# Optimization experiments

Hardware: AMD Instinct MI355X
Metric: run time of the kernel (lower is better)

The kernel has to match this reference:

```python
import jax, jax.numpy as jnp
import numpy as np

N = 100000   # nodes
E = 1000000  # directed edges
D = 64       # in_dim
H = 64       # hid_dim
O = 64       # out_dim


def _lin_init(key, fan_in, fan_out):
    # torch nn.Linear default init: U(-1/sqrt(fan_in), 1/sqrt(fan_in))
    k1, k2 = jax.random.split(key)
    s = 1.0 / np.sqrt(fan_in)
    W = jax.random.uniform(k1, (fan_in, fan_out), jnp.float32, -s, s)
    b = jax.random.uniform(k2, (fan_out,), jnp.float32, -s, s)
    return W, b


def setup_inputs() -> dict:
    key = jax.random.key(0)
    ks = jax.random.split(key, 6)
    x = jax.random.normal(ks[0], (N, D), jnp.float32)
    src = jax.random.randint(ks[1], (E,), 0, N)
    dst = jax.random.randint(ks[2], (E,), 0, N)
    W1, b1 = _lin_init(ks[3], 2 * D, H)
    W2, b2 = _lin_init(ks[4], 2 * H, H)
    W3, b3 = _lin_init(ks[5], 2 * H, O)
    return {"x": x, "src": src, "dst": dst,
            "W1": W1, "b1": b1, "W2": W2, "b2": b2, "W3": W3, "b3": b3}


def _graphconv_left(x, s, d, n):
    # DGL GraphConv(norm='left', weight=False, bias=False):
    # divide src features by src out-degree (clamped min 1), sum at dst.
    deg = jax.ops.segment_sum(jnp.ones_like(s, x.dtype), s, num_segments=n)
    deg = jnp.maximum(deg, 1.0)
    msg = (x / deg[:, None])[s]                       # [E, F] gather
    return jax.ops.segment_sum(msg, d, num_segments=n)  # [N, F] scatter-add


def _sage_layer(x, s, d, n, W, b, use_activation):
    agg = _graphconv_left(x, s, d, n)
    h = jnp.concatenate([x, agg], axis=1) @ W + b
    return jax.nn.relu(h) if use_activation else h


def reference(x, src, dst, W1, b1, W2, b2, W3, b3):
    n = x.shape[0]
    # dir_seq = 'OIU': out-edges, reversed edges, undirected (both directions)
    usrc = jnp.concatenate([src, dst])
    udst = jnp.concatenate([dst, src])
    x = _sage_layer(x, src, dst, n, W1, b1, True)    # 'O'
    x = _sage_layer(x, dst, src, n, W2, b2, True)    # 'I' (reverse graph)
    x = _sage_layer(x, usrc, udst, n, W3, b3, False) # 'U' (undirected)
    return x
```

## Files before the change

### kernel.cpp

```cpp
#include <hip/hip_runtime.h>
#include <hip/hip_fp16.h>


#define BSHIFT 10
#define BMASK  ((1 << BSHIFT) - 1)
#define NBMAX  128
#define PCHUNK 2048
#define HCHUNK 4096

__global__ __launch_bounds__(256) void bucket_hist_k(
    const int* __restrict__ src, const int* __restrict__ dst,
    int* __restrict__ bcnt_out, int* __restrict__ bcnt_in, int E) {
    __shared__ int h0[NBMAX], h1[NBMAX];
    const int t = threadIdx.x;
    const int e0 = blockIdx.x * HCHUNK;
    int n = E - e0; if (n > HCHUNK) n = HCHUNK;
    for (int i = t; i < NBMAX; i += 256) { h0[i] = 0; h1[i] = 0; }
    __syncthreads();
    for (int i = t; i < n; i += 256) {
        atomicAdd(&h0[src[e0 + i] >> BSHIFT], 1);
        atomicAdd(&h1[dst[e0 + i] >> BSHIFT], 1);
    }
    __syncthreads();
    if (t < NBMAX) {
        int c = h0[t];
        if (c) atomicAdd(&bcnt_out[t], c);
    } else {
        int b = t - NBMAX;
        int c = h1[b];
        if (c) atomicAdd(&bcnt_in[b], c);
    }
}

__global__ void bucket_scan_k(const int* __restrict__ bcnt_out, const int* __restrict__ bcnt_in,
                              int* __restrict__ bip_out, int* __restrict__ bip_in,
                              int* __restrict__ bcur_out, int* __restrict__ bcur_in, int NB) {
    __shared__ int s[1024];
    int t = threadIdx.x;
#pragma unroll 1
    for (int pass = 0; pass < 2; ++pass) {
        const int* bcnt = pass ? bcnt_in : bcnt_out;
        int* bip = pass ? bip_in : bip_out;
        int* bcur = pass ? bcur_in : bcur_out;
        int v = (t < NB) ? bcnt[t] : 0;
        s[t] = v; __syncthreads();
        for (int off = 1; off < 1024; off <<= 1) {
            int x = (t >= off) ? s[t - off] : 0;
            __syncthreads();
            s[t] += x;
            __syncthreads();
        }
        int excl = s[t] - v;
        if (t < NB) { bip[t] = excl; bcur[t] = excl; }
        if (t == NB) bip[NB] = excl;
        __syncthreads();
    }
}

__global__ __launch_bounds__(256) void partition_k(
    const int* __restrict__ src, const int* __restrict__ dst,
    int* __restrict__ bcur_out, int* __restrict__ bcur_in,
    unsigned* __restrict__ part_out, unsigned* __restrict__ part_in, int E) {
    __shared__ int sS[PCHUNK], sD[PCHUNK];
    __shared__ int hist[2][NBMAX];
    __shared__ int gbase[2][NBMAX];
    const int t = threadIdx.x;
    const int e0 = blockIdx.x * PCHUNK;
    int n = E - e0; if (n > PCHUNK) n = PCHUNK;

    for (int i = t; i < NBMAX; i += 256) { hist[0][i] = 0; hist[1][i] = 0; }
    __syncthreads();
    for (int i = t; i < n; i += 256) {
        int s = src[e0 + i], d = dst[e0 + i];
        sS[i] = s; sD[i] = d;
        atomicAdd(&hist[0][d >> BSHIFT], 1);
        atomicAdd(&hist[1][s >> BSHIFT], 1);
    }
    __syncthreads();
    if (t < NBMAX) {
        int c = hist[0][t];
        gbase[0][t] = c ? atomicAdd(&bcur_in[t], c) : 0;
        hist[0][t] = 0;
    } else {
        int b = t - NBMAX;
        int c = hist[1][b];
        gbase[1][b] = c ? atomicAdd(&bcur_out[b], c) : 0;
        hist[1][b] = 0;
    }
    __syncthreads();
    for (int i = t; i < n; i += 256) {
        int s = sS[i], d = sD[i];
        int bi = d >> BSHIFT;
        int p = gbase[0][bi] + atomicAdd(&hist[0][bi], 1);
        part_in[p] = ((unsigned)s << BSHIFT) | (unsigned)(d & BMASK);
        int bo = s >> BSHIFT;
        int q = gbase[1][bo] + atomicAdd(&hist[1][bo], 1);
        part_out[q] = ((unsigned)d << BSHIFT) | (unsigned)(s & BMASK);
    }
}

__global__ __launch_bounds__(1024) void bucket_sort_k(
    const unsigned* __restrict__ pa, const int* __restrict__ bipa,
    const unsigned* __restrict__ pb, const int* __restrict__ bipb,
    int* __restrict__ ipa, int* __restrict__ ipb,
    int* __restrict__ cola, int* __restrict__ colb,
    int* __restrict__ dega, int* __restrict__ degb, int N, int E) {
    const unsigned* part = blockIdx.y ? pb : pa;
    const int* bip = blockIdx.y ? bipb : bipa;
    int* ip  = blockIdx.y ? ipb : ipa;
    int* col = blockIdx.y ? colb : cola;
    int* deg = blockIdx.y ? degb : dega;
    __shared__ int cnt[1024];
    __shared__ int s[1024];
    const int g = blockIdx.x, t = threadIdx.x;
    const int b = bip[g], e = bip[g + 1];

    cnt[t] = 0;
    __syncthreads();
    for (int i = b + t; i < e; i += 1024) atomicAdd(&cnt[part[i] & (unsigned)BMASK], 1);
    __syncthreads();

    int v = cnt[t];
    s[t] = v;
    __syncthreads();
    for (int off = 1; off < 1024; off <<= 1) {
        int x = (t >= off) ? s[t - off] : 0;
        __syncthreads();
        s[t] += x;
        __syncthreads();
    }
    int base = b + s[t] - v;
    int node = (g << BSHIFT) + t;
    if (node < N) { ip[node] = base; deg[node] = v; }
    cnt[t] = base;
    if (g == 0 && t == 0) ip[N] = E;
    __syncthreads();
    for (int i = b + t; i < e; i += 1024) {
        unsigned rec = part[i];
        int p = atomicAdd(&cnt[rec & (unsigned)BMASK], 1);
        col[p] = (int)((rec >> BSHIFT) << 7);
    }
}

__global__ void scale_rows_k(const float* __restrict__ in, const int* __restrict__ deg,
                             __half* __restrict__ out, int n4) {
    int t = blockIdx.x * blockDim.x + threadIdx.x;
    if (t < n4) {
        int m = deg[t >> 4];
        float s = 1.0f / (float)(m < 1 ? 1 : m);
        float4 v = ((const float4*)in)[t];
        __half2 p01 = __floats2half2_rn(v.x * s, v.y * s);
        __half2 p23 = __floats2half2_rn(v.z * s, v.w * s);
        uint2 u;
        u.x = *(unsigned*)&p01;
        u.y = *(unsigned*)&p23;
        *(uint2*)(out + ((size_t)t << 2)) = u;
    }
}

__device__ __forceinline__ void acc_row(float4& acc, uint2 u) {
    __half2 h01 = *(__half2*)&u.x, h23 = *(__half2*)&u.y;
    acc.x += __low2float(h01); acc.y += __high2float(h01);
    acc.z += __low2float(h23); acc.w += __high2float(h23);
}

__device__ __forceinline__ void agg_list(const char* __restrict__ hsb,
                                         const int* __restrict__ col,
                                         int b, int e, int lane, int grp, int fo8,
                                         float4& a0, float4& a1, float4& a2, float4& a3) {
    for (int base = b; base < e; base += 64) {
        int cnt = e - base; if (cnt > 64) cnt = 64;
        int my = (lane < cnt) ? col[base + lane] : 0;
        for (int j = 0; j < cnt; j += 16) {
            int i0 = j + grp, i1 = j + 4 + grp, i2 = j + 8 + grp, i3 = j + 12 + grp;
            int o0 = __shfl(my, i0 < cnt ? i0 : 0);
            int o1 = __shfl(my, i1 < cnt ? i1 : 0);
            int o2 = __shfl(my, i2 < cnt ? i2 : 0);
            int o3 = __shfl(my, i3 < cnt ? i3 : 0);
            uint2 u0 = *(const uint2*)(hsb + o0 + fo8);
            uint2 u1 = *(const uint2*)(hsb + o1 + fo8);
            uint2 u2 = *(const uint2*)(hsb + o2 + fo8);
            uint2 u3 = *(const uint2*)(hsb + o3 + fo8);
            if (i0 < cnt) acc_row(a0, u0);
            if (i1 < cnt) acc_row(a1, u1);
            if (i2 < cnt) acc_row(a2, u2);
            if (i3 < cnt) acc_row(a3, u3);
        }
    }
}

__device__ __forceinline__ void agg_finish(float4 a0, float4 a1, float4 a2, float4 a3,
                                           float* __restrict__ agg, int node,
                                           int lane, int fo) {
    float4 acc;
    acc.x = (a0.x + a1.x) + (a2.x + a3.x);
    acc.y = (a0.y + a1.y) + (a2.y + a3.y);
    acc.z = (a0.z + a1.z) + (a2.z + a3.z);
    acc.w = (a0.w + a1.w) + (a2.w + a3.w);
    acc.x += __shfl_xor(acc.x, 16); acc.y += __shfl_xor(acc.y, 16);
    acc.z += __shfl_xor(acc.z, 16); acc.w += __shfl_xor(acc.w, 16);
    acc.x += __shfl_xor(acc.x, 32); acc.y += __shfl_xor(acc.y, 32);
    acc.z += __shfl_xor(acc.z, 32); acc.w += __shfl_xor(acc.w, 32);
    if (lane < 16) ((float4*)(agg + ((size_t)node << 6)))[fo] = acc;
}

__global__ void agg_k(const __half* __restrict__ hs, const int* __restrict__ ip,
                      const int* __restrict__ col, float* __restrict__ agg, int N) {
    int node = (blockIdx.x * blockDim.x + threadIdx.x) >> 6;
    int lane = threadIdx.x & 63;
    if (node >= N) return;
    const int grp = lane >> 4, fo = lane & 15, fo8 = fo << 3;
    float4 z = make_float4(0.f, 0.f, 0.f, 0.f);
    float4 a0 = z, a1 = z, a2 = z, a3 = z;
    agg_list((const char*)hs, col, ip[node], ip[node + 1], lane, grp, fo8, a0, a1, a2, a3);
    agg_finish(a0, a1, a2, a3, agg, node, lane, fo);
}

__global__ void agg_dual_k(const __half* __restrict__ hs,
                           const int* __restrict__ ipA, const int* __restrict__ colA,
                           const int* __restrict__ ipB, const int* __restrict__ colB,
                           float* __restrict__ agg, int N) {
    int node = (blockIdx.x * blockDim.x + threadIdx.x) >> 6;
    int lane = threadIdx.x & 63;
    if (node >= N) return;
    const int grp = lane >> 4, fo = lane & 15, fo8 = fo << 3;
    float4 z = make_float4(0.f, 0.f, 0.f, 0.f);
    float4 a0 = z, a1 = z, a2 = z, a3 = z;
    agg_list((const char*)hs, colA, ipA[node], ipA[node + 1], lane, grp, fo8, a0, a1, a2, a3);
    agg_list((const char*)hs, colB, ipB[node], ipB[node + 1], lane, grp, fo8, a0, a1, a2, a3);
    agg_finish(a0, a1, a2, a3, agg, node, lane, fo);
}

template <bool RELU, bool WRITE_HS, bool DEG2>
__global__ __launch_bounds__(256, 2) void gemm_cat_k(
    const float* X, const float* A,
    const float* __restrict__ W, const float* __restrict__ B,
    const int* __restrict__ dga, const int* __restrict__ dgb,
    __half* __restrict__ hs_out, float* out, int N) {
    __shared__ float sW[128 * 64];
    __shared__ float sX[64 * 64];
    __shared__ float sA[64 * 64];
    const int tid = threadIdx.x;

    for (int i = tid; i < 2048; i += 256) ((float4*)sW)[i] = ((const float4*)W)[i];

    const int row0 = blockIdx.x * 64;
    for (int i = tid; i < 1024; i += 256) {
        int r = i >> 4, c4 = (i & 15) << 2;
        int gr = row0 + r;
        float4 xv = make_float4(0.f, 0.f, 0.f, 0.f), av = xv;
        if (gr < N) {
            xv = ((const float4*)X)[(size_t)gr * 16 + (i & 15)];
            av = ((const float4*)A)[(size_t)gr * 16 + (i & 15)];
        }
        int sc = c4 ^ ((r & 12) << 1);
        *(float4*)&sX[(r << 6) + sc] = xv;
        *(float4*)&sA[(r << 6) + sc] = av;
    }
    __syncthreads();

    const int c0 = (tid & 15) << 2;
    const int r0 = (tid >> 4) << 2;
    const int sw = (r0 & 12) << 1;

    float4 bv = *(const float4*)(B + c0);
    float acc[4][4];
#pragma unroll
    for (int i = 0; i < 4; ++i) {
        acc[i][0] = bv.x; acc[i][1] = bv.y; acc[i][2] = bv.z; acc[i][3] = bv.w;
    }

#define GEMM_ROW(i, av)                                                       \
    acc[i][0] = fmaf(av.x, w0.x, acc[i][0]); acc[i][1] = fmaf(av.x, w0.y, acc[i][1]); \
    acc[i][2] = fmaf(av.x, w0.z, acc[i][2]); acc[i][3] = fmaf(av.x, w0.w, acc[i][3]); \
    acc[i][0] = fmaf(av.y, w1.x, acc[i][0]); acc[i][1] = fmaf(av.y, w1.y, acc[i][1]); \
    acc[i][2] = fmaf(av.y, w1.z, acc[i][2]); acc[i][3] = fmaf(av.y, w1.w, acc[i][3]); \
    acc[i][0] = fmaf(av.z, w2.x, acc[i][0]); acc[i][1] = fmaf(av.z, w2.y, acc[i][1]); \
    acc[i][2] = fmaf(av.z, w2.z, acc[i][2]); acc[i][3] = fmaf(av.z, w2.w, acc[i][3]); \
    acc[i][0] = fmaf(av.w, w3.x, acc[i][0]); acc[i][1] = fmaf(av.w, w3.y, acc[i][1]); \
    acc[i][2] = fmaf(av.w, w3.z, acc[i][2]); acc[i][3] = fmaf(av.w, w3.w, acc[i][3]);

#pragma unroll 4
    for (int kb = 0; kb < 64; kb += 4) {
        const int kx = kb ^ sw;
        float4 w0 = *(const float4*)&sW[((kb + 0) << 6) + c0];
        float4 w1 = *(const float4*)&sW[((kb + 1) << 6) + c0];
        float4 w2 = *(const float4*)&sW[((kb + 2) << 6) + c0];
        float4 w3 = *(const float4*)&sW[((kb + 3) << 6) + c0];
        float4 a0 = *(const float4*)&sX[((r0 + 0) << 6) + kx];
        float4 a1 = *(const float4*)&sX[((r0 + 1) << 6) + kx];
        float4 a2 = *(const float4*)&sX[((r0 + 2) << 6) + kx];
        float4 a3 = *(const float4*)&sX[((r0 + 3) << 6) + kx];
        GEMM_ROW(0, a0) GEMM_ROW(1, a1) GEMM_ROW(2, a2) GEMM_ROW(3, a3)
    }
#pragma unroll 4
    for (int kb = 0; kb < 64; kb += 4) {
        const int kx = kb ^ sw;
        float4 w0 = *(const float4*)&sW[((kb + 64) << 6) + c0];
        float4 w1 = *(const float4*)&sW[((kb + 65) << 6) + c0];
        float4 w2 = *(const float4*)&sW[((kb + 66) << 6) + c0];
        float4 w3 = *(const float4*)&sW[((kb + 67) << 6) + c0];
        float4 a0 = *(const float4*)&sA[((r0 + 0) << 6) + kx];
        float4 a1 = *(const float4*)&sA[((r0 + 1) << 6) + kx];
        float4 a2 = *(const float4*)&sA[((r0 + 2) << 6) + kx];
        float4 a3 = *(const float4*)&sA[((r0 + 3) << 6) + kx];
        GEMM_ROW(0, a0) GEMM_ROW(1, a1) GEMM_ROW(2, a2) GEMM_ROW(3, a3)
    }
#undef GEMM_ROW

#pragma unroll
    for (int i = 0; i < 4; ++i) {
        int gr = row0 + r0 + i;
        if (gr < N) {
            float4 o;
            o.x = RELU ? fmaxf(acc[i][0], 0.f) : acc[i][0];
            o.y = RELU ? fmaxf(acc[i][1], 0.f) : acc[i][1];
            o.z = RELU ? fmaxf(acc[i][2], 0.f) : acc[i][2];
            o.w = RELU ? fmaxf(acc[i][3], 0.f) : acc[i][3];
            *(float4*)(out + ((size_t)gr << 6) + c0) = o;
            if (WRITE_HS) {
                int m = dga[gr] + (DEG2 ? dgb[gr] : 0);
                float rr = 1.0f / (float)(m < 1 ? 1 : m);
                __half2 p01 = __floats2half2_rn(o.x * rr, o.y * rr);
                __half2 p23 = __floats2half2_rn(o.z * rr, o.w * rr);
                uint2 u;
                u.x = *(unsigned*)&p01;
                u.y = *(unsigned*)&p23;
                *(uint2*)(hs_out + ((size_t)gr << 6) + c0) = u;
            }
        }
    }
}

extern "C" void kernel_launch(void* const* d_in, const int* in_sizes, int n_in,
                              void* d_out, int out_size, void* d_ws, size_t ws_size,
                              hipStream_t stream) {
    const float* x  = (const float*)d_in[0];
    const int* src  = (const int*)d_in[1];
    const int* dst  = (const int*)d_in[2];
    const float* W1 = (const float*)d_in[3];
    const float* b1 = (const float*)d_in[4];
    const float* W2 = (const float*)d_in[5];
    const float* b2 = (const float*)d_in[6];
    const float* W3 = (const float*)d_in[7];
    const float* b3 = (const float*)d_in[8];

    const int N = in_sizes[0] / 64;
    const int E = in_sizes[1];
    const int NB = (N + BMASK) >> BSHIFT;

    float* bufH  = (float*)d_ws;
    __half* bufHS = (__half*)(bufH + (size_t)N * 64);
    int* deg_out = (int*)(bufHS + (size_t)N * 64);
    int* deg_in  = deg_out + N;
    int* ip_out  = deg_in + N;
    int* ip_in   = ip_out + (N + 1);
    int* bcnt_out = ip_in + (N + 1);
    int* bcnt_in  = bcnt_out + NB;
    int* bip_out  = bcnt_in + NB;
    int* bip_in   = bip_out + (NB + 1);
    int* bcur_out = bip_in + (NB + 1);
    int* bcur_in  = bcur_out + NB;
    unsigned* part_out = (unsigned*)(bcur_in + NB);
    unsigned* part_in  = part_out + E;
    int* col_out = (int*)(part_in + E);
    int* col_in  = col_out + E;

    float* aggB = (float*)d_out;

    const int TPB = 256;
    const int n4  = N * 16;
    const int g4  = (n4 + TPB - 1) / TPB;
    const int gAg = (int)(((size_t)N * 64 + TPB - 1) / TPB);
    const int gGm = (N + 63) / 64;
    const int gP  = (E + PCHUNK - 1) / PCHUNK;
    const int gH  = (E + HCHUNK - 1) / HCHUNK;

    hipMemsetAsync(bcnt_out, 0, 2 * (size_t)NB * sizeof(int), stream);
    bucket_hist_k<<<gH, TPB, 0, stream>>>(src, dst, bcnt_out, bcnt_in, E);
    bucket_scan_k<<<1, 1024, 0, stream>>>(bcnt_out, bcnt_in, bip_out, bip_in,
                                          bcur_out, bcur_in, NB);
    partition_k<<<gP, TPB, 0, stream>>>(src, dst, bcur_out, bcur_in,
                                        part_out, part_in, E);
    bucket_sort_k<<<dim3(NB, 2), 1024, 0, stream>>>(part_out, bip_out, part_in, bip_in,
                                                    ip_out, ip_in, col_out, col_in,
                                                    deg_out, deg_in, N, E);

    scale_rows_k<<<g4, TPB, 0, stream>>>(x, deg_out, bufHS, n4);
    agg_k<<<gAg, TPB, 0, stream>>>(bufHS, ip_in, col_in, aggB, N);
    gemm_cat_k<true, true, false><<<gGm, TPB, 0, stream>>>(x, aggB, W1, b1,
                                                           deg_in, nullptr, bufHS, bufH, N);

    agg_k<<<gAg, TPB, 0, stream>>>(bufHS, ip_out, col_out, aggB, N);
    gemm_cat_k<true, true, true><<<gGm, TPB, 0, stream>>>(bufH, aggB, W2, b2,
                                                          deg_in, deg_out, bufHS, bufH, N);

    agg_dual_k<<<gAg, TPB, 0, stream>>>(bufHS, ip_in, col_in, ip_out, col_out, aggB, N);
    gemm_cat_k<false, false, false><<<gGm, TPB, 0, stream>>>(bufH, aggB, W3, b3,
                                                             nullptr, nullptr, nullptr,
                                                             (float*)d_out, N);
}
```

Baseline: 293.9 us.

## Replace FP32 SIMT concat-GEMM with FP16 MFMA kernel and prepacked weights

Swaps the shared-memory FP32 FMA GEMM for a wave-level MFMA 16x16x32 fp16 kernel. A new prep kernel converts each weight matrix to fp16 once per call and packs it in the MFMA B-fragment layout, and each wave loads its A fragments straight from global memory with no LDS. The aim is to cut the ALU cost of the three dense layers. In exchange, inputs and weights are rounded to fp16, and the output stores become scalar and strided across lanes, which may hurt write coalescing.

```diff
diff --git a/kernel.cpp b/kernel.cpp
--- a/kernel.cpp
+++ b/kernel.cpp
@@ -7,6 +7,9 @@
 #define NBMAX  128
 #define PCHUNK 2048
 #define HCHUNK 4096
+
+typedef _Float16 half8 __attribute__((ext_vector_type(8)));
+typedef float floatx4 __attribute__((ext_vector_type(4)));
 
 __global__ __launch_bounds__(256) void bucket_hist_k(
     const int* __restrict__ src, const int* __restrict__ dst,
@@ -142,6 +145,21 @@
     }
 }
 
+__global__ void prep_w_k(const float* __restrict__ W1, const float* __restrict__ W2,
+                         const float* __restrict__ W3, __half* __restrict__ wt) {
+    const float* W = blockIdx.x == 0 ? W1 : (blockIdx.x == 1 ? W2 : W3);
+    __half* o = wt + (size_t)blockIdx.x * 8192;
+    for (int idx = threadIdx.x; idx < 8192; idx += 256) {
+        int j = idx & 7;
+        int l = (idx >> 3) & 63;
+        int f = idx >> 9;
+        int kq = f >> 2, ct = f & 3;
+        int k = (kq << 5) + ((l >> 4) << 3) + j;
+        int c = (ct << 4) + (l & 15);
+        o[idx] = __float2half(W[k * 64 + c]);
+    }
+}
+
 __global__ void scale_rows_k(const float* __restrict__ in, const int* __restrict__ deg,
                              __half* __restrict__ out, int n4) {
     int t = blockIdx.x * blockDim.x + threadIdx.x;
@@ -232,101 +250,72 @@
 }
 
 template <bool RELU, bool WRITE_HS, bool DEG2>
-__global__ __launch_bounds__(256, 2) void gemm_cat_k(
-    const float* X, const float* A,
-    const float* __restrict__ W, const float* __restrict__ B,
+__global__ __launch_bounds__(256) void gemm_mfma_k(
+    const float* X, const float* A, const __half* __restrict__ WT,
+    const float* __restrict__ B,
     const int* __restrict__ dga, const int* __restrict__ dgb,
     __half* __restrict__ hs_out, float* out, int N) {
-    __shared__ float sW[128 * 64];
-    __shared__ float sX[64 * 64];
-    __shared__ float sA[64 * 64];
     const int tid = threadIdx.x;
-
-    for (int i = tid; i < 2048; i += 256) ((float4*)sW)[i] = ((const float4*)W)[i];
-
-    const int row0 = blockIdx.x * 64;
-    for (int i = tid; i < 1024; i += 256) {
-        int r = i >> 4, c4 = (i & 15) << 2;
-        int gr = row0 + r;
-        float4 xv = make_float4(0.f, 0.f, 0.f, 0.f), av = xv;
-        if (gr < N) {
-            xv = ((const float4*)X)[(size_t)gr * 16 + (i & 15)];
-            av = ((const float4*)A)[(size_t)gr * 16 + (i & 15)];
+    const int w = tid >> 6, l = tid & 63;
+    const int lr = l & 15, lh = l >> 4;
+    const int row0 = blockIdx.x * 64 + (w << 4);
+    const int arow = row0 + lr;
+    const bool rok = arow < N;
+
+    half8 bf[4][4];
+#pragma unroll
+    for (int kq = 0; kq < 4; ++kq)
+#pragma unroll
+        for (int ct = 0; ct < 4; ++ct)
+            bf[kq][ct] = *(const half8*)(WT + ((((kq << 2) | ct) << 9) + (l << 3)));
+
+    half8 af[4];
+#pragma unroll
+    for (int kq = 0; kq < 4; ++kq) {
+        const float* src = (kq < 2) ? X : A;
+        int kbase = ((kq & 1) << 5) + (lh << 3);
+        float4 v0 = make_float4(0.f, 0.f, 0.f, 0.f), v1 = v0;
+        if (rok) {
+            v0 = *(const float4*)(src + ((size_t)arow << 6) + kbase);
+            v1 = *(const float4*)(src + ((size_t)arow << 6) + kbase + 4);
         }
-        int sc = c4 ^ ((r & 12) << 1);
-        *(float4*)&sX[(r << 6) + sc] = xv;
-        *(float4*)&sA[(r << 6) + sc] = av;
-    }
-    __syncthreads();
-
-    const int c0 = (tid & 15) << 2;
-    const int r0 = (tid >> 4) << 2;
-    const int sw = (r0 & 12) << 1;
-
-    float4 bv = *(const float4*)(B + c0);
-    float acc[4][4];
-#pragma unroll
-    for (int i = 0; i < 4; ++i) {
-        acc[i][0] = bv.x; acc[i][1] = bv.y; acc[i][2] = bv.z; acc[i][3] = bv.w;
-    }
-
-#define GEMM_ROW(i, av)                                                       \
-    acc[i][0] = fmaf(av.x, w0.x, acc[i][0]); acc[i][1] = fmaf(av.x, w0.y, acc[i][1]); \
-    acc[i][2] = fmaf(av.x, w0.z, acc[i][2]); acc[i][3] = fmaf(av.x, w0.w, acc[i][3]); \
-    acc[i][0] = fmaf(av.y, w1.x, acc[i][0]); acc[i][1] = fmaf(av.y, w1.y, acc[i][1]); \
-    acc[i][2] = fmaf(av.y, w1.z, acc[i][2]); acc[i][3] = fmaf(av.y, w1.w, acc[i][3]); \
-    acc[i][0] = fmaf(av.z, w2.x, acc[i][0]); acc[i][1] = fmaf(av.z, w2.y, acc[i][1]); \
-    acc[i][2] = fmaf(av.z, w2.z, acc[i][2]); acc[i][3] = fmaf(av.z, w2.w, acc[i][3]); \
-    acc[i][0] = fmaf(av.w, w3.x, acc[i][0]); acc[i][1] = fmaf(av.w, w3.y, acc[i][1]); \
-    acc[i][2] = fmaf(av.w, w3.z, acc[i][2]); acc[i][3] = fmaf(av.w, w3.w, acc[i][3]);
-
-#pragma unroll 4
-    for (int kb = 0; kb < 64; kb += 4) {
-        const int kx = kb ^ sw;
-        float4 w0 = *(const float4*)&sW[((kb + 0) << 6) + c0];
-        float4 w1 = *(const float4*)&sW[((kb + 1) << 6) + c0];
-        float4 w2 = *(const float4*)&sW[((kb + 2) << 6) + c0];
-        float4 w3 = *(const float4*)&sW[((kb + 3) << 6) + c0];
-        float4 a0 = *(const float4*)&sX[((r0 + 0) << 6) + kx];
-        float4 a1 = *(const float4*)&sX[((r0 + 1) << 6) + kx];
-        float4 a2 = *(const float4*)&sX[((r0 + 2) << 6) + kx];
-        float4 a3 = *(const float4*)&sX[((r0 + 3) << 6) + kx];
-        GEMM_ROW(0, a0) GEMM_ROW(1, a1) GEMM_ROW(2, a2) GEMM_ROW(3, a3)
-    }
-#pragma unroll 4
-    for (int kb = 0; kb < 64; kb += 4) {
-        const int kx = kb ^ sw;
-        float4 w0 = *(const float4*)&sW[((kb + 64) << 6) + c0];
-        float4 w1 = *(const float4*)&sW[((kb + 65) << 6) + c0];
-        float4 w2 = *(const float4*)&sW[((kb + 66) << 6) + c0];
-        float4 w3 = *(const float4*)&sW[((kb + 67) << 6) + c0];
-        float4 a0 = *(const float4*)&sA[((r0 + 0) << 6) + kx];
-        float4 a1 = *(const float4*)&sA[((r0 + 1) << 6) + kx];
-        float4 a2 = *(const float4*)&sA[((r0 + 2) << 6) + kx];
-        float4 a3 = *(const float4*)&sA[((r0 + 3) << 6) + kx];
-        GEMM_ROW(0, a0) GEMM_ROW(1, a1) GEMM_ROW(2, a2) GEMM_ROW(3, a3)
-    }
-#undef GEMM_ROW
-
-#pragma unroll
-    for (int i = 0; i < 4; ++i) {
-        int gr = row0 + r0 + i;
-        if (gr < N) {
-            float4 o;
-            o.x = RELU ? fmaxf(acc[i][0], 0.f) : acc[i][0];
-            o.y = RELU ? fmaxf(acc[i][1], 0.f) : acc[i][1];
-            o.z = RELU ? fmaxf(acc[i][2], 0.f) : acc[i][2];
-            o.w = RELU ? fmaxf(acc[i][3], 0.f) : acc[i][3];
-            *(float4*)(out + ((size_t)gr << 6) + c0) = o;
+        half8 a;
+        a[0] = (_Float16)v0.x; a[1] = (_Float16)v0.y;
+        a[2] = (_Float16)v0.z; a[3] = (_Float16)v0.w;
+        a[4] = (_Float16)v1.x; a[5] = (_Float16)v1.y;
+        a[6] = (_Float16)v1.z; a[7] = (_Float16)v1.w;
+        af[kq] = a;
+    }
+
+    floatx4 acc[4];
+#pragma unroll
+    for (int ct = 0; ct < 4; ++ct) {
+        float bb = B[(ct << 4) + lr];
+        acc[ct][0] = bb; acc[ct][1] = bb; acc[ct][2] = bb; acc[ct][3] = bb;
+    }
+
+#pragma unroll
+    for (int kq = 0; kq < 4; ++kq)
+#pragma unroll
+        for (int ct = 0; ct < 4; ++ct)
+            acc[ct] = __builtin_amdgcn_mfma_f32_16x16x32_f16(af[kq], bf[kq][ct], acc[ct], 0, 0, 0);
+
+#pragma unroll
+    for (int reg = 0; reg < 4; ++reg) {
+        int rw = row0 + (lh << 2) + reg;
+        if (rw < N) {
+            float rr = 1.0f;
             if (WRITE_HS) {
-                int m = dga[gr] + (DEG2 ? dgb[gr] : 0);
-                float rr = 1.0f / (float)(m < 1 ? 1 : m);
-                __half2 p01 = __floats2half2_rn(o.x * rr, o.y * rr);
-                __half2 p23 = __floats2half2_rn(o.z * rr, o.w * rr);
-                uint2 u;
-                u.x = *(unsigned*)&p01;
-                u.y = *(unsigned*)&p23;
-                *(uint2*)(hs_out + ((size_t)gr << 6) + c0) = u;
+                int m = dga[rw] + (DEG2 ? dgb[rw] : 0);
+                rr = 1.0f / (float)(m < 1 ? 1 : m);
+            }
+#pragma unroll
+            for (int ct = 0; ct < 4; ++ct) {
+                float v = acc[ct][reg];
+                if (RELU) v = fmaxf(v, 0.f);
+                out[((size_t)rw << 6) + (ct << 4) + lr] = v;
+                if (WRITE_HS)
+                    hs_out[((size_t)rw << 6) + (ct << 4) + lr] = __float2half(v * rr);
             }
         }
     }
@@ -365,6 +354,7 @@
     unsigned* part_in  = part_out + E;
     int* col_out = (int*)(part_in + E);
     int* col_in  = col_out + E;
+    __half* wt = (__half*)(((uintptr_t)(col_in + E) + 255) & ~(uintptr_t)255);
 
     float* aggB = (float*)d_out;
 
@@ -377,6 +367,7 @@
     const int gH  = (E + HCHUNK - 1) / HCHUNK;
 
     hipMemsetAsync(bcnt_out, 0, 2 * (size_t)NB * sizeof(int), stream);
+    prep_w_k<<<3, TPB, 0, stream>>>(W1, W2, W3, wt);
     bucket_hist_k<<<gH, TPB, 0, stream>>>(src, dst, bcnt_out, bcnt_in, E);
     bucket_scan_k<<<1, 1024, 0, stream>>>(bcnt_out, bcnt_in, bip_out, bip_in,
                                           bcur_out, bcur_in, NB);
@@ -388,15 +379,15 @@
 
     scale_rows_k<<<g4, TPB, 0, stream>>>(x, deg_out, bufHS, n4);
     agg_k<<<gAg, TPB, 0, stream>>>(bufHS, ip_in, col_in, aggB, N);
-    gemm_cat_k<true, true, false><<<gGm, TPB, 0, stream>>>(x, aggB, W1, b1,
-                                                           deg_in, nullptr, bufHS, bufH, N);
+    gemm_mfma_k<true, true, false><<<gGm, TPB, 0, stream>>>(x, aggB, wt, b1,
+                                                            deg_in, nullptr, bufHS, bufH, N);
 
     agg_k<<<gAg, TPB, 0, stream>>>(bufHS, ip_out, col_out, aggB, N);
-    gemm_cat_k<true, true, true><<<gGm, TPB, 0, stream>>>(bufH, aggB, W2, b2,
-                                                          deg_in, deg_out, bufHS, bufH, N);
+    gemm_mfma_k<true, true, true><<<gGm, TPB, 0, stream>>>(bufH, aggB, wt + 8192, b2,
+                                                           deg_in, deg_out, bufHS, bufH, N);
 
     agg_dual_k<<<gAg, TPB, 0, stream>>>(bufHS, ip_in, col_in, ip_out, col_out, aggB, N);
-    gemm_cat_k<false, false, false><<<gGm, TPB, 0, stream>>>(bufH, aggB, W3, b3,
-                                                             nullptr, nullptr, nullptr,
-                                                             (float*)d_out, N);
-}
+    gemm_mfma_k<false, false, false><<<gGm, TPB, 0, stream>>>(bufH, aggB, wt + 16384, b3,
+                                                              nullptr, nullptr, nullptr,
+                                                              (float*)d_out, N);
+}
```

New measurement: 251.7 us. 1.17x faster.
